# Kernel tuning notes

Hardware: AMD Instinct MI355X
Metric: run time of the kernel (lower is better)

The kernel has to match this reference:

```python
import jax, jax.numpy as jnp
import numpy as np

N_NODES = 50000
N_EDGES = 600000
D = 128


def setup_inputs() -> dict:
    key = jax.random.key(0)
    k1, k2, k3, k4, k5, k6 = jax.random.split(key, 6)
    h = jax.random.normal(k1, (N_NODES, D), dtype=jnp.float32)
    e_h = jax.random.normal(k2, (N_EDGES, D), dtype=jnp.float32)
    norm = jax.random.uniform(k3, (N_NODES, 1), dtype=jnp.float32)
    dst = jax.random.randint(k4, (N_EDGES,), 0, N_NODES)
    # nn.Linear(in_hid=128, out_hid=128) weight/bias
    W = jax.random.normal(k5, (D, D), dtype=jnp.float32) * (1.0 / np.sqrt(D))
    b = jax.random.normal(k6, (D,), dtype=jnp.float32) * 0.01
    return {"h": h, "e_h": e_h, "norm": norm, "dst": dst, "W": W, "b": b}


def reference(h, e_h, norm, dst, W, b):
    # DGL fn.v_mul_e: message per edge = h[dst] * e_h  (elementwise)
    msg = h[dst] * e_h                                    # [E, D]
    # fn.sum: scatter-sum messages to destination nodes
    agg = jax.ops.segment_sum(msg, dst, num_segments=N_NODES)  # [N, D]
    # apply_func: linear projection, then per-node norm scaling
    out = agg @ W.T + b                                   # [N, D]
    out = out * norm                                      # broadcast [N,1]
    # dropout is identity in eval mode; activation is None by default
    return out
```

## Files before the change

### kernel.cpp

```cpp
#include <hip/hip_runtime.h>

#define N_NODES 50000
#define N_EDGES 600000
#define D 128
#define TILE_N 32
#define SCAN_B 1024
#define N_SCAN_BLOCKS ((N_NODES + SCAN_B - 1) / SCAN_B)

typedef float f4 __attribute__((ext_vector_type(4)));


__global__ __launch_bounds__(256) void hist_kernel(
    const int* __restrict__ dst, int* __restrict__ cnt)
{
    int e = blockIdx.x * 256 + threadIdx.x;
    if (e < N_EDGES) atomicAdd(&cnt[dst[e]], 1);
}

__global__ __launch_bounds__(SCAN_B) void scan_sum_kernel(
    const int* __restrict__ cnt, int* __restrict__ partial)
{
    int t = threadIdx.x;
    int i = blockIdx.x * SCAN_B + t;
    int v = (i < N_NODES) ? cnt[i] : 0;
#pragma unroll
    for (int s = 32; s > 0; s >>= 1) v += __shfl_down(v, s, 64);
    __shared__ int wsum[SCAN_B / 64];
    if ((t & 63) == 0) wsum[t >> 6] = v;
    __syncthreads();
    if (t < SCAN_B / 64) {
        int x = wsum[t];
#pragma unroll
        for (int s = SCAN_B / 128; s > 0; s >>= 1) x += __shfl_down(x, s, SCAN_B / 64);
        if (t == 0) partial[blockIdx.x] = x;
    }
}

__global__ __launch_bounds__(64) void scan_partial_kernel(int* __restrict__ partial)
{
    int t = threadIdx.x;
    int v = (t < N_SCAN_BLOCKS) ? partial[t] : 0;
    int own = v;
#pragma unroll
    for (int s = 1; s < 64; s <<= 1) {
        int u = __shfl_up(v, s, 64);
        if (t >= s) v += u;
    }
    if (t < N_SCAN_BLOCKS) partial[t] = v - own;
}

__global__ __launch_bounds__(SCAN_B) void scan_emit_kernel(
    const int* __restrict__ cnt, const int* __restrict__ partial,
    int* __restrict__ offsets, int* __restrict__ cursor)
{
    int t = threadIdx.x;
    int i = blockIdx.x * SCAN_B + t;
    int v = (i < N_NODES) ? cnt[i] : 0;
    __shared__ int sd[SCAN_B];
    sd[t] = v;
    __syncthreads();
    for (int s = 1; s < SCAN_B; s <<= 1) {
        int u = (t >= s) ? sd[t - s] : 0;
        __syncthreads();
        sd[t] += u;
        __syncthreads();
    }
    int excl = sd[t] - v + partial[blockIdx.x];
    if (i < N_NODES) { offsets[i] = excl; cursor[i] = excl; }
    if (i == N_NODES - 1) offsets[N_NODES] = excl + v;
}

__global__ __launch_bounds__(256) void fill_kernel(
    const int* __restrict__ dst, int* __restrict__ cursor,
    int* __restrict__ edge_ids)
{
    int e = blockIdx.x * 256 + threadIdx.x;
    if (e < N_EDGES) {
        int pos = atomicAdd(&cursor[dst[e]], 1);
        edge_ids[pos] = e;
    }
}

__global__ __launch_bounds__(256) void agg_kernel(
    const float* __restrict__ h, const float* __restrict__ e_h,
    const int* __restrict__ offsets, const int* __restrict__ edge_ids,
    float* __restrict__ A)
{
    int gid  = blockIdx.x * 256 + threadIdx.x;
    int node = gid >> 5;
    int lane = gid & 31;
    if (node >= N_NODES) return;

    const int beg = offsets[node];
    const int end = offsets[node + 1];
    const int fo  = lane << 2;

    f4 acc = (f4){0.f, 0.f, 0.f, 0.f};

    int i = beg;
    const int n4 = beg + ((end - beg) & ~3);

    if (i < n4) {
        int id0 = edge_ids[i + 0];
        int id1 = edge_ids[i + 1];
        int id2 = edge_ids[i + 2];
        int id3 = edge_ids[i + 3];
        i += 4;
        for (; i < n4; i += 4) {
            int j0 = edge_ids[i + 0];
            int j1 = edge_ids[i + 1];
            int j2 = edge_ids[i + 2];
            int j3 = edge_ids[i + 3];
            f4 v0 = __builtin_nontemporal_load((const f4*)(e_h + (size_t)id0 * D + fo));
            f4 v1 = __builtin_nontemporal_load((const f4*)(e_h + (size_t)id1 * D + fo));
            f4 v2 = __builtin_nontemporal_load((const f4*)(e_h + (size_t)id2 * D + fo));
            f4 v3 = __builtin_nontemporal_load((const f4*)(e_h + (size_t)id3 * D + fo));
            acc += (v0 + v1) + (v2 + v3);
            id0 = j0; id1 = j1; id2 = j2; id3 = j3;
        }
        f4 v0 = __builtin_nontemporal_load((const f4*)(e_h + (size_t)id0 * D + fo));
        f4 v1 = __builtin_nontemporal_load((const f4*)(e_h + (size_t)id1 * D + fo));
        f4 v2 = __builtin_nontemporal_load((const f4*)(e_h + (size_t)id2 * D + fo));
        f4 v3 = __builtin_nontemporal_load((const f4*)(e_h + (size_t)id3 * D + fo));
        acc += (v0 + v1) + (v2 + v3);
    }
    if (i < end) {
        int id = edge_ids[i];
        for (; i < end; ++i) {
            int nid = (i + 1 < end) ? edge_ids[i + 1] : 0;
            f4 v = __builtin_nontemporal_load((const f4*)(e_h + (size_t)id * D + fo));
            acc += v;
            id = nid;
        }
    }

    f4 hv = *(const f4*)(h + (size_t)node * D + fo);
    acc *= hv;
    *(f4*)(A + (size_t)node * D + fo) = acc;
}

__global__ __launch_bounds__(256, 2) void gemm_from_A(
    const float* __restrict__ A, const float* __restrict__ norm,
    const float* __restrict__ W, const float* __restrict__ b,
    float* __restrict__ out)
{
    __shared__ float Wl[D * D];
    __shared__ float Al[TILE_N * D];
    const int tid = threadIdx.x;
    const int n0  = blockIdx.x * TILE_N;

    for (int it = 0; it < 16; ++it) {
        int group = it * 256 + tid;
        int c  = group >> 5;
        int kg = group & 31;
        float4 wv = *(const float4*)(W + (size_t)c * D + (kg << 2));
        int g = (kg + c) & 31;
        *(float4*)(Wl + c * D + (g << 2)) = wv;
    }
    for (int it = 0; it < 4; ++it) {
        int group = it * 256 + tid;
        int nl = group >> 5;
        int f  = (group & 31) << 2;
        int n  = n0 + nl;
        float4 a = make_float4(0.f, 0.f, 0.f, 0.f);
        if (n < N_NODES) a = *(const float4*)(A + (size_t)n * D + f);
        *(float4*)(Al + nl * D + f) = a;
    }
    __syncthreads();

    const int cg = tid & 31;
    const int ng = tid >> 5;
    float facc[4][4];
#pragma unroll
    for (int i = 0; i < 4; ++i)
#pragma unroll
        for (int j = 0; j < 4; ++j) facc[i][j] = 0.f;

#pragma unroll 4
    for (int kc = 0; kc < 32; ++kc) {
        float4 a[4];
#pragma unroll
        for (int i = 0; i < 4; ++i)
            a[i] = *(const float4*)(Al + (ng * 4 + i) * D + (kc << 2));
        float4 w[4];
#pragma unroll
        for (int j = 0; j < 4; ++j) {
            int c = cg + 32 * j;
            int g = (kc + c) & 31;
            w[j] = *(const float4*)(Wl + c * D + (g << 2));
        }
#pragma unroll
        for (int i = 0; i < 4; ++i)
#pragma unroll
            for (int j = 0; j < 4; ++j)
                facc[i][j] += a[i].x * w[j].x + a[i].y * w[j].y +
                              a[i].z * w[j].z + a[i].w * w[j].w;
    }
    float bias[4];
#pragma unroll
    for (int j = 0; j < 4; ++j) bias[j] = b[cg + 32 * j];
#pragma unroll
    for (int i = 0; i < 4; ++i) {
        int n = n0 + ng * 4 + i;
        if (n >= N_NODES) break;
        float nv = norm[n];
#pragma unroll
        for (int j = 0; j < 4; ++j)
            out[(size_t)n * D + cg + 32 * j] = (facc[i][j] + bias[j]) * nv;
    }
}

__global__ __launch_bounds__(256) void scatter_kernel(
    const float* __restrict__ e_h, const int* __restrict__ dst,
    float* __restrict__ S)
{
    long long idx = (long long)blockIdx.x * 256 + threadIdx.x;
    int edge = (int)(idx >> 5);
    if (edge >= N_EDGES) return;
    int f = ((int)idx & 31) << 2;
    const float4 v = *(const float4*)(e_h + (size_t)edge * D + f);
    float* p = S + (size_t)dst[edge] * D + f;
    atomicAdd(p + 0, v.x);
    atomicAdd(p + 1, v.y);
    atomicAdd(p + 2, v.z);
    atomicAdd(p + 3, v.w);
}

__global__ __launch_bounds__(256, 2) void gemm_kernel(
    const float* __restrict__ h, const float* __restrict__ S,
    const float* __restrict__ norm, const float* __restrict__ W,
    const float* __restrict__ b, float* __restrict__ out)
{
    __shared__ float Wl[D * D];
    __shared__ float Al[TILE_N * D];
    const int tid = threadIdx.x;
    const int n0  = blockIdx.x * TILE_N;

    for (int it = 0; it < 16; ++it) {
        int group = it * 256 + tid;
        int c  = group >> 5;
        int kg = group & 31;
        float4 wv = *(const float4*)(W + (size_t)c * D + (kg << 2));
        int g = (kg + c) & 31;
        *(float4*)(Wl + c * D + (g << 2)) = wv;
    }
    for (int it = 0; it < 4; ++it) {
        int group = it * 256 + tid;
        int nl = group >> 5;
        int f  = (group & 31) << 2;
        int n  = n0 + nl;
        float4 a = make_float4(0.f, 0.f, 0.f, 0.f);
        if (n < N_NODES) {
            float4 hv = *(const float4*)(h + (size_t)n * D + f);
            float4 sv = *(const float4*)(S + (size_t)n * D + f);
            a = make_float4(hv.x * sv.x, hv.y * sv.y, hv.z * sv.z, hv.w * sv.w);
        }
        *(float4*)(Al + nl * D + f) = a;
    }
    __syncthreads();

    const int cg = tid & 31;
    const int ng = tid >> 5;
    float facc[4][4];
#pragma unroll
    for (int i = 0; i < 4; ++i)
#pragma unroll
        for (int j = 0; j < 4; ++j) facc[i][j] = 0.f;

#pragma unroll 4
    for (int kc = 0; kc < 32; ++kc) {
        float4 a[4];
#pragma unroll
        for (int i = 0; i < 4; ++i)
            a[i] = *(const float4*)(Al + (ng * 4 + i) * D + (kc << 2));
        float4 w[4];
#pragma unroll
        for (int j = 0; j < 4; ++j) {
            int c = cg + 32 * j;
            int g = (kc + c) & 31;
            w[j] = *(const float4*)(Wl + c * D + (g << 2));
        }
#pragma unroll
        for (int i = 0; i < 4; ++i)
#pragma unroll
            for (int j = 0; j < 4; ++j)
                facc[i][j] += a[i].x * w[j].x + a[i].y * w[j].y +
                              a[i].z * w[j].z + a[i].w * w[j].w;
    }
    float bias[4];
#pragma unroll
    for (int j = 0; j < 4; ++j) bias[j] = b[cg + 32 * j];
#pragma unroll
    for (int i = 0; i < 4; ++i) {
        int n = n0 + ng * 4 + i;
        if (n >= N_NODES) break;
        float nv = norm[n];
#pragma unroll
        for (int j = 0; j < 4; ++j)
            out[(size_t)n * D + cg + 32 * j] = (facc[i][j] + bias[j]) * nv;
    }
}

extern "C" void kernel_launch(void* const* d_in, const int* in_sizes, int n_in,
                              void* d_out, int out_size, void* d_ws, size_t ws_size,
                              hipStream_t stream) {
    const float* h    = (const float*)d_in[0];
    const float* e_h  = (const float*)d_in[1];
    const float* norm = (const float*)d_in[2];
    const int*   dst  = (const int*)d_in[3];
    const float* W    = (const float*)d_in[4];
    const float* b    = (const float*)d_in[5];
    float* out = (float*)d_out;

    const size_t ints_needed = (size_t)N_NODES + (N_NODES + 1) + N_EDGES + 64;
    const size_t full_bytes  = ints_needed * sizeof(int) + (size_t)N_NODES * D * sizeof(float);

    if (ws_size >= full_bytes) {
        int* cursor   = (int*)d_ws;
        int* offsets  = cursor + N_NODES;
        int* edge_ids = offsets + N_NODES + 1;
        int* partial  = edge_ids + N_EDGES;
        float* A      = (float*)(partial + 64);

        hipMemsetAsync(cursor, 0, (size_t)N_NODES * sizeof(int), stream);

        int eblocks = (N_EDGES + 255) / 256;
        hist_kernel<<<eblocks, 256, 0, stream>>>(dst, cursor);
        scan_sum_kernel<<<N_SCAN_BLOCKS, SCAN_B, 0, stream>>>(cursor, partial);
        scan_partial_kernel<<<1, 64, 0, stream>>>(partial);
        scan_emit_kernel<<<N_SCAN_BLOCKS, SCAN_B, 0, stream>>>(cursor, partial,
                                                               offsets, cursor);
        fill_kernel<<<eblocks, 256, 0, stream>>>(dst, cursor, edge_ids);

        int ablocks = ((N_NODES * 32) + 255) / 256;
        agg_kernel<<<ablocks, 256, 0, stream>>>(h, e_h, offsets, edge_ids, A);

        int gblocks = (N_NODES + TILE_N - 1) / TILE_N;
        gemm_from_A<<<gblocks, 256, 0, stream>>>(A, norm, W, b, out);
    } else {
        const size_t s_bytes = (size_t)N_NODES * D * sizeof(float);
        float* S = (ws_size >= s_bytes) ? (float*)d_ws : out;
        hipMemsetAsync(S, 0, s_bytes, stream);
        int scatter_blocks = (N_EDGES * 32 + 255) / 256;
        scatter_kernel<<<scatter_blocks, 256, 0, stream>>>(e_h, dst, S);
        int gemm_blocks = (N_NODES + TILE_N - 1) / TILE_N;
        gemm_kernel<<<gemm_blocks, 256, 0, stream>>>(h, S, norm, W, b, out);
    }
}
```

Measured before the change: 175.2 us.

## Fuse aggregation into GEMM tile and merge scan into single-pass decoupled scan

```diff
diff --git a/kernel.cpp b/kernel.cpp
--- a/kernel.cpp
+++ b/kernel.cpp
@@ -17,55 +17,62 @@
     if (e < N_EDGES) atomicAdd(&cnt[dst[e]], 1);
 }
 
-__global__ __launch_bounds__(SCAN_B) void scan_sum_kernel(
-    const int* __restrict__ cnt, int* __restrict__ partial)
-{
-    int t = threadIdx.x;
-    int i = blockIdx.x * SCAN_B + t;
-    int v = (i < N_NODES) ? cnt[i] : 0;
-#pragma unroll
-    for (int s = 32; s > 0; s >>= 1) v += __shfl_down(v, s, 64);
+__global__ __launch_bounds__(SCAN_B) void scan_kernel(
+    const int* __restrict__ cnt, unsigned long long* __restrict__ desc,
+    int* __restrict__ offsets, int* __restrict__ cursor)
+{
+    const int t  = threadIdx.x;
+    const int bx = blockIdx.x;
+    const int i  = bx * SCAN_B + t;
+    const int v  = (i < N_NODES) ? cnt[i] : 0;
+
+    const int lane = t & 63;
+    const int w    = t >> 6;
+    int incl = v;
+#pragma unroll
+    for (int s = 1; s < 64; s <<= 1) {
+        int u = __shfl_up(incl, s, 64);
+        if (lane >= s) incl += u;
+    }
     __shared__ int wsum[SCAN_B / 64];
-    if ((t & 63) == 0) wsum[t >> 6] = v;
+    if (lane == 63) wsum[w] = incl;
     __syncthreads();
     if (t < SCAN_B / 64) {
         int x = wsum[t];
 #pragma unroll
-        for (int s = SCAN_B / 128; s > 0; s >>= 1) x += __shfl_down(x, s, SCAN_B / 64);
-        if (t == 0) partial[blockIdx.x] = x;
-    }
-}
-
-__global__ __launch_bounds__(64) void scan_partial_kernel(int* __restrict__ partial)
-{
-    int t = threadIdx.x;
-    int v = (t < N_SCAN_BLOCKS) ? partial[t] : 0;
-    int own = v;
-#pragma unroll
-    for (int s = 1; s < 64; s <<= 1) {
-        int u = __shfl_up(v, s, 64);
-        if (t >= s) v += u;
-    }
-    if (t < N_SCAN_BLOCKS) partial[t] = v - own;
-}
-
-__global__ __launch_bounds__(SCAN_B) void scan_emit_kernel(
-    const int* __restrict__ cnt, const int* __restrict__ partial,
-    int* __restrict__ offsets, int* __restrict__ cursor)
-{
-    int t = threadIdx.x;
-    int i = blockIdx.x * SCAN_B + t;
-    int v = (i < N_NODES) ? cnt[i] : 0;
-    __shared__ int sd[SCAN_B];
-    sd[t] = v;
-    __syncthreads();
-    for (int s = 1; s < SCAN_B; s <<= 1) {
-        int u = (t >= s) ? sd[t - s] : 0;
-        __syncthreads();
-        sd[t] += u;
-        __syncthreads();
-    }
-    int excl = sd[t] - v + partial[blockIdx.x];
+        for (int s = 1; s < SCAN_B / 64; s <<= 1) {
+            int u = __shfl_up(x, s, SCAN_B / 64);
+            if (t >= s) x += u;
+        }
+        wsum[t] = x;
+    }
+    __syncthreads();
+    const int block_total   = wsum[SCAN_B / 64 - 1];
+    const int excl_in_block = (w ? wsum[w - 1] : 0) + (incl - v);
+
+    if (t == 0)
+        __hip_atomic_store(&desc[bx],
+            (unsigned long long)(unsigned)block_total | (1ull << 63),
+            __ATOMIC_RELEASE, __HIP_MEMORY_SCOPE_AGENT);
+
+    __shared__ int base_sh;
+    if (t < 64) {
+        int pred = 0;
+        if (t < bx) {
+            unsigned long long e;
+            do {
+                e = __hip_atomic_load(&desc[t], __ATOMIC_ACQUIRE,
+                                      __HIP_MEMORY_SCOPE_AGENT);
+            } while (!(e >> 63));
+            pred = (int)(unsigned)e;
+        }
+#pragma unroll
+        for (int s = 32; s > 0; s >>= 1) pred += __shfl_down(pred, s, 64);
+        if (t == 0) base_sh = pred;
+    }
+    __syncthreads();
+
+    const int excl = base_sh + excl_in_block;
     if (i < N_NODES) { offsets[i] = excl; cursor[i] = excl; }
     if (i == N_NODES - 1) offsets[N_NODES] = excl + v;
 }
@@ -81,68 +88,11 @@
     }
 }
 
-__global__ __launch_bounds__(256) void agg_kernel(
+__global__ __launch_bounds__(256, 2) void fused_tile(
     const float* __restrict__ h, const float* __restrict__ e_h,
     const int* __restrict__ offsets, const int* __restrict__ edge_ids,
-    float* __restrict__ A)
-{
-    int gid  = blockIdx.x * 256 + threadIdx.x;
-    int node = gid >> 5;
-    int lane = gid & 31;
-    if (node >= N_NODES) return;
-
-    const int beg = offsets[node];
-    const int end = offsets[node + 1];
-    const int fo  = lane << 2;
-
-    f4 acc = (f4){0.f, 0.f, 0.f, 0.f};
-
-    int i = beg;
-    const int n4 = beg + ((end - beg) & ~3);
-
-    if (i < n4) {
-        int id0 = edge_ids[i + 0];
-        int id1 = edge_ids[i + 1];
-        int id2 = edge_ids[i + 2];
-        int id3 = edge_ids[i + 3];
-        i += 4;
-        for (; i < n4; i += 4) {
-            int j0 = edge_ids[i + 0];
-            int j1 = edge_ids[i + 1];
-            int j2 = edge_ids[i + 2];
-            int j3 = edge_ids[i + 3];
-            f4 v0 = __builtin_nontemporal_load((const f4*)(e_h + (size_t)id0 * D + fo));
-            f4 v1 = __builtin_nontemporal_load((const f4*)(e_h + (size_t)id1 * D + fo));
-            f4 v2 = __builtin_nontemporal_load((const f4*)(e_h + (size_t)id2 * D + fo));
-            f4 v3 = __builtin_nontemporal_load((const f4*)(e_h + (size_t)id3 * D + fo));
-            acc += (v0 + v1) + (v2 + v3);
-            id0 = j0; id1 = j1; id2 = j2; id3 = j3;
-        }
-        f4 v0 = __builtin_nontemporal_load((const f4*)(e_h + (size_t)id0 * D + fo));
-        f4 v1 = __builtin_nontemporal_load((const f4*)(e_h + (size_t)id1 * D + fo));
-        f4 v2 = __builtin_nontemporal_load((const f4*)(e_h + (size_t)id2 * D + fo));
-        f4 v3 = __builtin_nontemporal_load((const f4*)(e_h + (size_t)id3 * D + fo));
-        acc += (v0 + v1) + (v2 + v3);
-    }
-    if (i < end) {
-        int id = edge_ids[i];
-        for (; i < end; ++i) {
-            int nid = (i + 1 < end) ? edge_ids[i + 1] : 0;
-            f4 v = __builtin_nontemporal_load((const f4*)(e_h + (size_t)id * D + fo));
-            acc += v;
-            id = nid;
-        }
-    }
-
-    f4 hv = *(const f4*)(h + (size_t)node * D + fo);
-    acc *= hv;
-    *(f4*)(A + (size_t)node * D + fo) = acc;
-}
-
-__global__ __launch_bounds__(256, 2) void gemm_from_A(
-    const float* __restrict__ A, const float* __restrict__ norm,
-    const float* __restrict__ W, const float* __restrict__ b,
-    float* __restrict__ out)
+    const float* __restrict__ norm, const float* __restrict__ W,
+    const float* __restrict__ b, float* __restrict__ out)
 {
     __shared__ float Wl[D * D];
     __shared__ float Al[TILE_N * D];
@@ -157,14 +107,57 @@
         int g = (kg + c) & 31;
         *(float4*)(Wl + c * D + (g << 2)) = wv;
     }
-    for (int it = 0; it < 4; ++it) {
-        int group = it * 256 + tid;
-        int nl = group >> 5;
-        int f  = (group & 31) << 2;
-        int n  = n0 + nl;
-        float4 a = make_float4(0.f, 0.f, 0.f, 0.f);
-        if (n < N_NODES) a = *(const float4*)(A + (size_t)n * D + f);
-        *(float4*)(Al + nl * D + f) = a;
+
+    const int grp  = tid >> 5;
+    const int lane = tid & 31;
+    const int fo   = lane << 2;
+
+    for (int s = 0; s < 4; ++s) {
+        const int nl = grp * 4 + s;
+        const int n  = n0 + nl;
+        f4 acc = (f4){0.f, 0.f, 0.f, 0.f};
+        if (n < N_NODES) {
+            const int beg = offsets[n];
+            const int end = offsets[n + 1];
+            int i = beg;
+            const int n4 = beg + ((end - beg) & ~3);
+            if (i < n4) {
+                int id0 = edge_ids[i + 0];
+                int id1 = edge_ids[i + 1];
+                int id2 = edge_ids[i + 2];
+                int id3 = edge_ids[i + 3];
+                i += 4;
+                for (; i < n4; i += 4) {
+                    int j0 = edge_ids[i + 0];
+                    int j1 = edge_ids[i + 1];
+                    int j2 = edge_ids[i + 2];
+                    int j3 = edge_ids[i + 3];
+                    f4 v0 = __builtin_nontemporal_load((const f4*)(e_h + (size_t)id0 * D + fo));
+                    f4 v1 = __builtin_nontemporal_load((const f4*)(e_h + (size_t)id1 * D + fo));
+                    f4 v2 = __builtin_nontemporal_load((const f4*)(e_h + (size_t)id2 * D + fo));
+                    f4 v3 = __builtin_nontemporal_load((const f4*)(e_h + (size_t)id3 * D + fo));
+                    acc += (v0 + v1) + (v2 + v3);
+                    id0 = j0; id1 = j1; id2 = j2; id3 = j3;
+                }
+                f4 v0 = __builtin_nontemporal_load((const f4*)(e_h + (size_t)id0 * D + fo));
+                f4 v1 = __builtin_nontemporal_load((const f4*)(e_h + (size_t)id1 * D + fo));
+                f4 v2 = __builtin_nontemporal_load((const f4*)(e_h + (size_t)id2 * D + fo));
+                f4 v3 = __builtin_nontemporal_load((const f4*)(e_h + (size_t)id3 * D + fo));
+                acc += (v0 + v1) + (v2 + v3);
+            }
+            if (i < end) {
+                int id = edge_ids[i];
+                for (; i < end; ++i) {
+                    int nid = (i + 1 < end) ? edge_ids[i + 1] : 0;
+                    f4 v = __builtin_nontemporal_load((const f4*)(e_h + (size_t)id * D + fo));
+                    acc += v;
+                    id = nid;
+                }
+            }
+            f4 hv = *(const f4*)(h + (size_t)n * D + fo);
+            acc *= hv;
+        }
+        *(f4*)(Al + nl * D + fo) = acc;
     }
     __syncthreads();
 
@@ -312,31 +305,26 @@
     const float* b    = (const float*)d_in[5];
     float* out = (float*)d_out;
 
-    const size_t ints_needed = (size_t)N_NODES + (N_NODES + 1) + N_EDGES + 64;
-    const size_t full_bytes  = ints_needed * sizeof(int) + (size_t)N_NODES * D * sizeof(float);
+    const size_t ints_needed = (size_t)N_NODES + 128 + (N_NODES + 1) + N_EDGES;
+    const size_t full_bytes  = ints_needed * sizeof(int);
 
     if (ws_size >= full_bytes) {
         int* cursor   = (int*)d_ws;
-        int* offsets  = cursor + N_NODES;
+        unsigned long long* desc = (unsigned long long*)(cursor + N_NODES);
+        int* offsets  = cursor + N_NODES + 128;
         int* edge_ids = offsets + N_NODES + 1;
-        int* partial  = edge_ids + N_EDGES;
-        float* A      = (float*)(partial + 64);
-
-        hipMemsetAsync(cursor, 0, (size_t)N_NODES * sizeof(int), stream);
+
+        hipMemsetAsync(cursor, 0, ((size_t)N_NODES + 128) * sizeof(int), stream);
 
         int eblocks = (N_EDGES + 255) / 256;
         hist_kernel<<<eblocks, 256, 0, stream>>>(dst, cursor);
-        scan_sum_kernel<<<N_SCAN_BLOCKS, SCAN_B, 0, stream>>>(cursor, partial);
-        scan_partial_kernel<<<1, 64, 0, stream>>>(partial);
-        scan_emit_kernel<<<N_SCAN_BLOCKS, SCAN_B, 0, stream>>>(cursor, partial,
-                                                               offsets, cursor);
+        scan_kernel<<<N_SCAN_BLOCKS, SCAN_B, 0, stream>>>(cursor, desc,
+                                                          offsets, cursor);
         fill_kernel<<<eblocks, 256, 0, stream>>>(dst, cursor, edge_ids);
 
-        int ablocks = ((N_NODES * 32) + 255) / 256;
-        agg_kernel<<<ablocks, 256, 0, stream>>>(h, e_h, offsets, edge_ids, A);
-
         int gblocks = (N_NODES + TILE_N - 1) / TILE_N;
-        gemm_from_A<<<gblocks, 256, 0, stream>>>(A, norm, W, b, out);
+        fused_tile<<<gblocks, 256, 0, stream>>>(h, e_h, offsets, edge_ids,
+                                                norm, W, b, out);
     } else {
         const size_t s_bytes = (size_t)N_NODES * D * sizeof(float);
         float* S = (ws_size >= s_bytes) ? (float*)d_ws : out;
```

Result: slower. 193.4 us (+10.4%).
